# Optimization experiments

Hardware: AMD Instinct MI355X
Metric: run time of the kernel (lower is better)

## Reference

```python
import jax, jax.numpy as jnp
import numpy as np

NUM_CLASSES = 1_000_000
EMBED_DIM = 64
NEG_NUM = 512
TEMPERATURE = 1.0
B, T = 32, 128


def setup_inputs() -> dict:
    key = jax.random.key(0)
    k1, k2, k3, k4, k5 = jax.random.split(key, 5)
    embeds = jax.random.normal(k1, (B, T, EMBED_DIM), dtype=jnp.float32)
    labels = jax.random.randint(k2, (B, T), 0, NUM_CLASSES, dtype=jnp.int64)
    neg_samples = jax.random.randint(k3, (B * T, NEG_NUM), 0, NUM_CLASSES, dtype=jnp.int64)
    proj_w = jax.random.normal(k4, (EMBED_DIM, EMBED_DIM), dtype=jnp.float32) / np.sqrt(EMBED_DIM)
    proj_b = jnp.zeros((EMBED_DIM,), dtype=jnp.float32)
    emb_table = jax.random.normal(k5, (NUM_CLASSES, EMBED_DIM), dtype=jnp.float32)
    return {"embeds": embeds, "labels": labels, "neg_samples": neg_samples,
            "proj_w": proj_w, "proj_b": proj_b, "emb_table": emb_table}


def reference(embeds, labels, neg_samples, proj_w, proj_b, emb_table):
    # projector: Linear(D, D). torch Linear: x @ W.T + b; here proj_w stored as [D_in, D_out].
    x = jnp.einsum('btd,de->bte', embeds, proj_w) + proj_b
    # all labels are valid (!= Env.null), so target extraction = flatten [B*T, D]
    target_x = x.reshape(-1, EMBED_DIM)            # [N, D]
    target_y = labels.reshape(-1)                  # [N]
    pos_embs = emb_table[target_y]                 # [N, D] gather
    neg_embs = emb_table[neg_samples]              # [N, K, D] gather
    pos_score = jnp.einsum('nd,nd->n', target_x, pos_embs)[:, None]   # [N, 1]
    neg_score = jnp.einsum('nd,nkd->nk', target_x, neg_embs)          # [N, K]
    logits = jnp.concatenate([pos_score, neg_score], axis=1)          # [N, 1+K]
    scaled = logits / TEMPERATURE
    # cross_entropy with labels == 0 everywhere
    loss = jnp.mean(jax.nn.logsumexp(scaled, axis=1) - scaled[:, 0])
    return logits, loss
```

## Files before the change

kernel.cpp:

```cpp
#include <hip/hip_runtime.h>
#include <hip/hip_bf16.h>

#define N_TOK 4096
#define EMB_D 64
#define NEG_K 512
#define LOGITS_W 513

__global__ __launch_bounds__(256) void proj_kernel(
    const float* __restrict__ embeds,
    const float* __restrict__ W,
    const float* __restrict__ b,
    float* __restrict__ x,
    float* __restrict__ loss)
{
    __shared__ float Ws[EMB_D][EMB_D];
    __shared__ float Es[4][EMB_D];
    const int tid = threadIdx.x;
    const int n0 = blockIdx.x * 4;

    for (int i = tid; i < EMB_D * EMB_D; i += 256)
        Ws[i >> 6][i & 63] = W[i];
    for (int i = tid; i < 4 * EMB_D; i += 256)
        Es[i >> 6][i & 63] = embeds[(size_t)n0 * EMB_D + i];
    __syncthreads();

    const int nl = tid >> 6;
    const int e  = tid & 63;
    float acc = b[e];
    #pragma unroll
    for (int d = 0; d < EMB_D; ++d)
        acc += Es[nl][d] * Ws[d][e];
    x[(size_t)(n0 + nl) * EMB_D + e] = acc;

    if (blockIdx.x == 0 && tid == 0) loss[0] = 0.0f;
}

__global__ __launch_bounds__(512) void score_kernel(
    const float* __restrict__ x,
    const int*   __restrict__ labels,
    const int*   __restrict__ neg,
    const float* __restrict__ table,
    float* __restrict__ logits,
    float* __restrict__ loss)
{
    const int n   = blockIdx.x;
    const int tid = threadIdx.x;

    __shared__ float xs[EMB_D];
    __shared__ float red[8];
    __shared__ float posS;
    __shared__ float Ms;

    if (tid < EMB_D) xs[tid] = x[(size_t)n * EMB_D + tid];
    __syncthreads();

    const float4* xv = (const float4*)xs;

    const int idx = neg[(size_t)n * NEG_K + tid];
    const float4* row = (const float4*)(table + (size_t)idx * EMB_D);
    float acc = 0.0f;
    #pragma unroll
    for (int j = 0; j < 16; ++j) {
        float4 r = row[j];
        float4 v = xv[j];
        acc += r.x * v.x + r.y * v.y + r.z * v.z + r.w * v.w;
    }
    logits[(size_t)n * LOGITS_W + 1 + tid] = acc;

    if (tid < 16) {
        const int pidx = labels[n];
        const float4* prow = (const float4*)(table + (size_t)pidx * EMB_D);
        float4 r = prow[tid];
        float4 v = xv[tid];
        float p = r.x * v.x + r.y * v.y + r.z * v.z + r.w * v.w;
        #pragma unroll
        for (int o = 8; o > 0; o >>= 1) p += __shfl_xor(p, o, 16);
        if (tid == 0) {
            posS = p;
            logits[(size_t)n * LOGITS_W] = p;
        }
    }
    __syncthreads();
    const float pos = posS;

    float m = acc;
    #pragma unroll
    for (int o = 32; o > 0; o >>= 1) m = fmaxf(m, __shfl_xor(m, o));
    const int wave = tid >> 6;
    if ((tid & 63) == 0) red[wave] = m;
    __syncthreads();
    if (tid == 0) {
        float mm = pos;
        #pragma unroll
        for (int w = 0; w < 8; ++w) mm = fmaxf(mm, red[w]);
        Ms = mm;
    }
    __syncthreads();
    const float M = Ms;

    float e = expf(acc - M);
    #pragma unroll
    for (int o = 32; o > 0; o >>= 1) e += __shfl_xor(e, o);
    __syncthreads();
    if ((tid & 63) == 0) red[wave] = e;
    __syncthreads();
    if (tid == 0) {
        float s = expf(pos - M);
        #pragma unroll
        for (int w = 0; w < 8; ++w) s += red[w];
        const float lse = M + logf(s);
        atomicAdd(loss, (lse - pos) * (1.0f / (float)N_TOK));
    }
}

extern "C" void kernel_launch(void* const* d_in, const int* in_sizes, int n_in,
                              void* d_out, int out_size, void* d_ws, size_t ws_size,
                              hipStream_t stream) {
    const float* embeds = (const float*)d_in[0];
    const int*   labels = (const int*)d_in[1];
    const int*   neg    = (const int*)d_in[2];
    const float* proj_w = (const float*)d_in[3];
    const float* proj_b = (const float*)d_in[4];
    const float* table  = (const float*)d_in[5];

    float* logits = (float*)d_out;
    float* loss   = (float*)d_out + (size_t)N_TOK * LOGITS_W;
    float* x      = (float*)d_ws;

    proj_kernel<<<N_TOK / 4, 256, 0, stream>>>(embeds, proj_w, proj_b, x, loss);
    score_kernel<<<N_TOK, 512, 0, stream>>>(x, labels, neg, table, logits, loss);
}
```

Before: 104.4 us.

## Gather table rows cooperatively with 16 lanes per row and stage logits in LDS

Each negative row is now read by 16 lanes, each loading one float4, so a wavefront's row loads become contiguous 256-byte segments. Previously one thread streamed a whole row on its own, giving scattered per-thread access. Dot products are reduced with 16-lane shuffles, and scores are staged in shared memory so the logits row is written contiguously. The cost is extra shuffle reductions and LDS traffic.

```diff
diff --git a/kernel.cpp b/kernel.cpp
--- a/kernel.cpp
+++ b/kernel.cpp
@@ -45,66 +45,69 @@
 {
     const int n   = blockIdx.x;
     const int tid = threadIdx.x;
+    const int g   = tid >> 4;
+    const int l   = tid & 15;
 
     __shared__ float xs[EMB_D];
+    __shared__ int   nidx[NEG_K];
+    __shared__ float sc[LOGITS_W];
     __shared__ float red[8];
-    __shared__ float posS;
     __shared__ float Ms;
 
+    nidx[tid] = neg[(size_t)n * NEG_K + tid];
     if (tid < EMB_D) xs[tid] = x[(size_t)n * EMB_D + tid];
     __syncthreads();
 
-    const float4* xv = (const float4*)xs;
-
-    const int idx = neg[(size_t)n * NEG_K + tid];
-    const float4* row = (const float4*)(table + (size_t)idx * EMB_D);
-    float acc = 0.0f;
-    #pragma unroll
-    for (int j = 0; j < 16; ++j) {
-        float4 r = row[j];
-        float4 v = xv[j];
-        acc += r.x * v.x + r.y * v.y + r.z * v.z + r.w * v.w;
-    }
-    logits[(size_t)n * LOGITS_W + 1 + tid] = acc;
+    const float4 xr = ((const float4*)xs)[l];
 
     if (tid < 16) {
         const int pidx = labels[n];
-        const float4* prow = (const float4*)(table + (size_t)pidx * EMB_D);
-        float4 r = prow[tid];
-        float4 v = xv[tid];
-        float p = r.x * v.x + r.y * v.y + r.z * v.z + r.w * v.w;
+        const float4 r = ((const float4*)(table + (size_t)pidx * EMB_D))[l];
+        float p = r.x * xr.x + r.y * xr.y + r.z * xr.z + r.w * xr.w;
         #pragma unroll
         for (int o = 8; o > 0; o >>= 1) p += __shfl_xor(p, o, 16);
-        if (tid == 0) {
-            posS = p;
-            logits[(size_t)n * LOGITS_W] = p;
-        }
+        if (tid == 0) sc[0] = p;
+    }
+
+    #pragma unroll
+    for (int i = 0; i < 16; ++i) {
+        const int k   = i * 32 + g;
+        const int idx = nidx[k];
+        const float4 r = ((const float4*)(table + (size_t)idx * EMB_D))[l];
+        float p = r.x * xr.x + r.y * xr.y + r.z * xr.z + r.w * xr.w;
+        #pragma unroll
+        for (int o = 8; o > 0; o >>= 1) p += __shfl_xor(p, o, 16);
+        if (l == 0) sc[1 + k] = p;
     }
     __syncthreads();
-    const float pos = posS;
 
-    float m = acc;
+    const float v = sc[1 + tid];
+    float m = (tid == 0) ? fmaxf(v, sc[0]) : v;
     #pragma unroll
     for (int o = 32; o > 0; o >>= 1) m = fmaxf(m, __shfl_xor(m, o));
     const int wave = tid >> 6;
     if ((tid & 63) == 0) red[wave] = m;
     __syncthreads();
     if (tid == 0) {
-        float mm = pos;
+        float mm = red[0];
         #pragma unroll
-        for (int w = 0; w < 8; ++w) mm = fmaxf(mm, red[w]);
+        for (int w = 1; w < 8; ++w) mm = fmaxf(mm, red[w]);
         Ms = mm;
     }
     __syncthreads();
     const float M = Ms;
 
-    float e = expf(acc - M);
+    float e = expf(v - M);
     #pragma unroll
     for (int o = 32; o > 0; o >>= 1) e += __shfl_xor(e, o);
     __syncthreads();
     if ((tid & 63) == 0) red[wave] = e;
     __syncthreads();
+
+    logits[(size_t)n * LOGITS_W + tid] = sc[tid];
     if (tid == 0) {
+        logits[(size_t)n * LOGITS_W + 512] = sc[512];
+        const float pos = sc[0];
         float s = expf(pos - M);
         #pragma unroll
         for (int w = 0; w < 8; ++w) s += red[w];
```

Measured after the change: 109.6 us. 1.05x slower.
